# Kernel tuning notes

Hardware: AMD Instinct MI355X
Metric: run time of the kernel (lower is better)

Reference implementation:

```python
import jax, jax.numpy as jnp
import numpy as np

TAU = 1.0
EPS = 1e-5


def _gcn_sparse(x, src, dst, ew, W, b, n):
    # PyG GCNConv: add self-loops (weight 1), sym-normalize, aggregate src->dst
    deg = jax.ops.segment_sum(ew, dst, num_segments=n) + 1.0
    dinv = jnp.where(deg > 0, jax.lax.rsqrt(deg), 0.0)
    h = x @ W
    coef = dinv[src] * ew * dinv[dst]              # [E]
    out = jax.ops.segment_sum(h[src] * coef[:, None], dst, num_segments=n)
    out = out + h * (dinv * dinv)[:, None]         # self-loop term
    return out + b


def _gcn_dense(x, A, W, b):
    # x: [B,N,d], A: [B,N,N] with A[b,i,j] = weight of edge j->i
    n = A.shape[-1]
    Ah = A + jnp.eye(n, dtype=A.dtype)
    deg = Ah.sum(-1)
    dinv = jnp.where(deg > 0, jax.lax.rsqrt(deg), 0.0)
    An = dinv[:, :, None] * Ah * dinv[:, None, :]
    return jnp.einsum('bij,bjd->bid', An, x @ W) + b


def _bn_silu(x, g, be, axes):
    # BatchNorm over node axis (training-mode batch stats, biased var) + SiLU
    m = x.mean(axes, keepdims=True)
    v = x.var(axes, keepdims=True)
    return jax.nn.silu(g * (x - m) * jax.lax.rsqrt(v + EPS) + be)


def setup_inputs() -> dict:
    key = jax.random.key(0)
    ks = jax.random.split(key, 12)
    B, NPG, EPER = 32, 1024, 16384
    CIN, C, K1, K2, OUT = 64, 128, 128, 32, 10
    N, E = B * NPG, B * EPER
    ei = jax.random.randint(ks[0], (2, E), 0, NPG, dtype=jnp.int32)
    off = jnp.repeat(jnp.arange(B, dtype=jnp.int32) * NPG, EPER)
    edge_index = ei + off[None, :]
    x = jax.random.normal(ks[1], (N, CIN), jnp.float32)
    batch = jnp.repeat(jnp.arange(B, dtype=jnp.int32), NPG)
    batch_ptr = jnp.arange(B + 1, dtype=jnp.int32) * NPG
    p = lambda k, s: jax.random.normal(k, s, jnp.float32) * 0.05
    return dict(
        x=x, edge_index=edge_index, batch=batch, batch_ptr=batch_ptr,
        w1a=p(ks[2], (CIN, C)), b1a=jnp.zeros((C,)), g1a=jnp.ones((C,)), be1a=jnp.zeros((C,)),
        w1b=p(ks[3], (C, C)), b1b=jnp.zeros((C,)), g1b=jnp.ones((C,)), be1b=jnp.zeros((C,)),
        wp1=p(ks[4], (C, K1)), bp1=jnp.zeros((K1,)),
        w2a=p(ks[5], (C, C)), b2a=jnp.zeros((C,)), g2a=jnp.ones((C,)), be2a=jnp.zeros((C,)),
        w2b=p(ks[6], (C, C)), b2b=jnp.zeros((C,)), g2b=jnp.ones((C,)), be2b=jnp.zeros((C,)),
        wp2=p(ks[7], (C, K2)), bp2=jnp.zeros((K2,)),
        wl=p(ks[8], (C, OUT)), bl=jnp.zeros((OUT,)))


def reference(x, edge_index, batch, batch_ptr,
              w1a, b1a, g1a, be1a, w1b, b1b, g1b, be1b, wp1, bp1,
              w2a, b2a, g2a, be2a, w2b, b2b, g2b, be2b, wp2, bp2,
              wl, bl):
    n = x.shape[0]
    B = batch_ptr.shape[0] - 1
    npg = n // B                                    # uniform nodes per graph
    src, dst = edge_index[0], edge_index[1]
    ew = jnp.ones((edge_index.shape[1],), x.dtype)  # edge_weight=None -> ones

    # ---- stack 1: sparse GCN residual blocks + stochastic pool ----
    h = _bn_silu(_gcn_sparse(x, src, dst, ew, w1a, b1a, n), g1a, be1a, 0)
    h = h + _bn_silu(_gcn_sparse(h, src, dst, ew, w1b, b1b, n), g1b, be1b, 0)
    s = jax.nn.softmax(_gcn_sparse(h, src, dst, ew, wp1, bp1, n) / TAU, -1)  # [n,K1]
    s3 = s.reshape(B, npg, -1)
    x2 = jnp.einsum('bnc,bnd->bcd', s3, h.reshape(B, npg, -1))   # s^T x  [B,K1,C]
    t = jax.ops.segment_sum(s[src] * ew[:, None], dst, num_segments=n)  # A s
    A2 = jnp.einsum('bnc,bnk->bck', s3, t.reshape(B, npg, -1))   # s^T A s [B,K1,K1]

    # ---- stack 2: dense GCN on pooled graph + stochastic pool ----
    h2 = _bn_silu(_gcn_dense(x2, A2, w2a, b2a), g2a, be2a, (0, 1))
    h2 = h2 + _bn_silu(_gcn_dense(h2, A2, w2b, b2b), g2b, be2b, (0, 1))
    s2 = jax.nn.softmax(_gcn_dense(h2, A2, wp2, bp2) / TAU, -1)  # [B,K1,K2]
    x3 = jnp.einsum('bnc,bnd->bcd', s2, h2)                      # [B,K2,C]

    # global mean pool over nodes per graph, linear, log_softmax
    g = x3.mean(axis=1)
    out = jax.nn.log_softmax(g @ wl + bl, axis=1)
    # aux losses are multiplied by 0 in the original forward -> exact zero
    return (out, jnp.zeros((), x.dtype))
```

## Files before the change

kernel.cpp:

```cpp
#include <hip/hip_runtime.h>
#include <cmath>

#define KSPLIT 8
#define ELL_ST 80

typedef __attribute__((ext_vector_type(8))) short short8;
typedef __attribute__((ext_vector_type(4))) float float4v;

static __device__ __forceinline__ unsigned short f2bf(float f){
  union { float f; unsigned u; } c; c.f = f;
  unsigned r = c.u + 0x7fff + ((c.u >> 16) & 1);
  return (unsigned short)(r >> 16);
}
static __device__ __forceinline__ float u2f(unsigned u){
  union { unsigned u; float f; } c; c.u = u; return c.f;
}
static __device__ __forceinline__ float silu(float y){ return y/(1.f+__expf(-y)); }

static __device__ __forceinline__ void coef_prologue(const float* __restrict__ stats,
                                                     const float* __restrict__ gamma,
                                                     const float* __restrict__ beta,
                                                     float invM, float* lds, int tbase){
  int t = threadIdx.x - tbase;
  if(t >= 0 && t < 128){
    float s = 0.f, q = 0.f;
    #pragma unroll
    for(int k=0;k<8;k++){ s += stats[k*128+t]; q += stats[1024 + k*128+t]; }
    float m = s*invM;
    float v = q*invM - m*m;
    float sc = gamma[t]*rsqrtf(v + 1e-5f);
    lds[t] = sc;
    lds[128+t] = beta[t] - m*sc;
  }
}

__global__ void k_fill_ell(const int* __restrict__ src, const int* __restrict__ dst,
                           int* __restrict__ cursor, int* __restrict__ esrc, int E){
  int e = blockIdx.x*256 + threadIdx.x;
  if(e<E){
    int d = dst[e];
    int p = atomicAdd(&cursor[d], 1);
    if(p < ELL_ST) esrc[(size_t)d*ELL_ST + p] = src[e];
  }
}

__global__ void k_dinv_wt(const int* __restrict__ deg, float* __restrict__ dinv, int n,
                          const float* __restrict__ w1a, const float* __restrict__ w1b,
                          const float* __restrict__ wp1, unsigned short* __restrict__ t1a,
                          unsigned short* __restrict__ t1b, unsigned short* __restrict__ tp1,
                          int CIN){
  int i = blockIdx.x*256 + threadIdx.x;
  if(i < n){ dinv[i] = rsqrtf((float)deg[i] + 1.0f); }
  int j = i - n;
  int n1 = CIN*128, n2 = 128*128;
  if(j >= 0 && j < n1){
    int k = j >> 7, c = j & 127;
    t1a[(size_t)c*CIN + k] = f2bf(w1a[j]);
  } else if(j >= n1 && j < n1+n2){
    int jj = j - n1; int k = jj >> 7, c = jj & 127;
    t1b[(size_t)c*128 + k] = f2bf(w1b[jj]);
  } else if(j >= n1+n2 && j < n1+2*n2){
    int jj = j - n1 - n2; int k = jj >> 7, c = jj & 127;
    tp1[(size_t)c*128 + k] = f2bf(wp1[jj]);
  }
}

__global__ void k_gemm_mfma(const float* __restrict__ A, const float* __restrict__ A2,
                            const unsigned short* __restrict__ Bt,
                            unsigned short* __restrict__ Cb, int M, int K, int Nc,
                            const float* __restrict__ rowscale,
                            const float* __restrict__ stA, const float* __restrict__ gA,
                            const float* __restrict__ beA,
                            const float* __restrict__ stB, const float* __restrict__ gB,
                            const float* __restrict__ beB, float invM){
  __shared__ unsigned short Abf[64][40];
  __shared__ unsigned short Bbf[64][40];
  __shared__ float lcA[256], lcB[256];
  int tid = threadIdx.x;
  if(stA) coef_prologue(stA, gA, beA, invM, lcA, 0);
  if(stB) coef_prologue(stB, gB, beB, invM, lcB, 128);
  if(stA || stB) __syncthreads();
  int wv = tid >> 6, lane = tid & 63;
  int quad = lane >> 4, l16 = lane & 15;
  int row0 = blockIdx.y*64, col0 = blockIdx.x*64;
  int sr = tid >> 2, sk = (tid & 3)*8;
  float4v acc[4] = {};
  for(int kt=0; kt<K; kt+=32){
    const float* ap = &A[(size_t)(row0+sr)*K + kt + sk];
    float va[8];
    *(float4*)&va[0] = *(const float4*)ap;
    *(float4*)&va[4] = *(const float4*)(ap+4);
    if(stB){
      const float* bp = &A2[(size_t)(row0+sr)*K + kt + sk];
      float vb[8];
      *(float4*)&vb[0] = *(const float4*)bp;
      *(float4*)&vb[4] = *(const float4*)(bp+4);
      #pragma unroll
      for(int i=0;i<8;i++){
        int c = kt+sk+i;
        va[i] = silu(lcA[c]*va[i] + lcA[128+c]) + silu(lcB[c]*vb[i] + lcB[128+c]);
      }
    } else if(stA){
      #pragma unroll
      for(int i=0;i<8;i++){
        int c = kt+sk+i;
        va[i] = silu(lcA[c]*va[i] + lcA[128+c]);
      }
    }
    uint4 pk;
    pk.x = (unsigned)f2bf(va[0]) | ((unsigned)f2bf(va[1])<<16);
    pk.y = (unsigned)f2bf(va[2]) | ((unsigned)f2bf(va[3])<<16);
    pk.z = (unsigned)f2bf(va[4]) | ((unsigned)f2bf(va[5])<<16);
    pk.w = (unsigned)f2bf(va[6]) | ((unsigned)f2bf(va[7])<<16);
    *(uint4*)&Abf[sr][sk] = pk;
    *(uint4*)&Bbf[sr][sk] = *(const uint4*)&Bt[(size_t)(col0+sr)*K + kt + sk];
    __syncthreads();
    short8 af = *(const short8*)&Abf[wv*16 + l16][quad*8];
    #pragma unroll
    for(int t=0;t<4;t++){
      short8 bf = *(const short8*)&Bbf[t*16 + l16][quad*8];
      acc[t] = __builtin_amdgcn_mfma_f32_16x16x32_bf16(af, bf, acc[t], 0, 0, 0);
    }
    __syncthreads();
  }
  float scr[4];
  #pragma unroll
  for(int r=0;r<4;r++){
    int grow = row0 + wv*16 + quad*4 + r;
    scr[r] = rowscale ? rowscale[grow] : 1.f;
  }
  #pragma unroll
  for(int t=0;t<4;t++){
    #pragma unroll
    for(int r=0;r<4;r++){
      int grow = row0 + wv*16 + quad*4 + r;
      int gcol = col0 + t*16 + l16;
      Cb[(size_t)grow*Nc + gcol] = f2bf(acc[t][r]*scr[r]);
    }
  }
}

__global__ void k_gemm64(const float* __restrict__ A, const float* __restrict__ B,
                         float* __restrict__ C, int M, int K, int Nc,
                         const float* __restrict__ rowscale,
                         const float* __restrict__ stA, const float* __restrict__ gA,
                         const float* __restrict__ beA, float invM){
  __shared__ float As[16][68];
  __shared__ float Bs[16][68];
  __shared__ float lc[256];
  int tid = threadIdx.x;
  if(stA){ coef_prologue(stA, gA, beA, invM, lc, 0); __syncthreads(); }
  int tx = tid & 15, ty = tid >> 4;
  int row0 = blockIdx.y*64, col0 = blockIdx.x*64;
  float acc[4][4] = {};
  for(int kt=0; kt<K; kt+=16){
    int ra = tid >> 2, ka = (tid & 3)*4;
    float4 va = *(const float4*)&A[(size_t)(row0+ra)*K + kt + ka];
    if(stA){
      float vv[4] = {va.x, va.y, va.z, va.w};
      #pragma unroll
      for(int i=0;i<4;i++){
        int c = kt+ka+i;
        vv[i] = silu(lc[c]*vv[i] + lc[128+c]);
      }
      va.x=vv[0]; va.y=vv[1]; va.z=vv[2]; va.w=vv[3];
    }
    As[ka+0][ra]=va.x; As[ka+1][ra]=va.y; As[ka+2][ra]=va.z; As[ka+3][ra]=va.w;
    int rb = tid >> 4, cb = (tid & 15)*4;
    *(float4*)&Bs[rb][cb] = *(const float4*)&B[(size_t)(kt+rb)*Nc + col0 + cb];
    __syncthreads();
    #pragma unroll
    for(int k=0;k<16;k++){
      float4 a = *(const float4*)&As[k][ty*4];
      float4 b = *(const float4*)&Bs[k][tx*4];
      float av[4]={a.x,a.y,a.z,a.w}, bv[4]={b.x,b.y,b.z,b.w};
      #pragma unroll
      for(int i=0;i<4;i++)
        #pragma unroll
        for(int j=0;j<4;j++) acc[i][j] += av[i]*bv[j];
    }
    __syncthreads();
  }
  #pragma unroll
  for(int i=0;i<4;i++){
    int r = row0 + ty*4 + i;
    float sc = rowscale ? rowscale[r] : 1.0f;
    float4 v; v.x=acc[i][0]*sc; v.y=acc[i][1]*sc; v.z=acc[i][2]*sc; v.w=acc[i][3]*sc;
    *(float4*)&C[(size_t)r*Nc + col0 + tx*4] = v;
  }
}

template<bool DO_SOFTMAX, bool GCN, bool STATS, bool BF16IN>
__global__ void k_gather(const int* __restrict__ degc, const int* __restrict__ esrc,
                         const float* __restrict__ dinv, const void* __restrict__ hWs,
                         const float* __restrict__ bias, float* __restrict__ out,
                         float* __restrict__ stats){
  __shared__ float lsum[4][128];
  __shared__ float lsq[4][128];
  const unsigned short* h16 = (const unsigned short*)hWs;
  const float* h32 = (const float*)hWs;
  int wave = threadIdx.x >> 6;
  int lane = threadIdx.x & 63;
  int bid = blockIdx.x;
  int d = ((bid & 7) << 12) | ((bid >> 3) << 2) | wave;
  int grp = lane >> 5;
  int c4 = (lane & 31)*4;
  int cnt = degc[d]; if(cnt > ELL_ST) cnt = ELL_ST;
  cnt = __builtin_amdgcn_readfirstlane(cnt);
  const int* row = esrc + (size_t)d*ELL_ST;

  auto loadrow = [&](int s)->float4{
    if(BF16IN){
      uint2 u = *(const uint2*)&h16[(size_t)s*128 + c4];
      float4 v;
      v.x = u2f(u.x << 16); v.y = u2f(u.x & 0xffff0000u);
      v.z = u2f(u.y << 16); v.w = u2f(u.y & 0xffff0000u);
      return v;
    } else {
      return *(const float4*)&h32[(size_t)s*128 + c4];
    }
  };

  float4 a0 = {0.f,0.f,0.f,0.f}, a1 = {0.f,0.f,0.f,0.f};
  float4 a2 = {0.f,0.f,0.f,0.f}, a3 = {0.f,0.f,0.f,0.f};
  if(GCN && grp == 0)
    a0 = loadrow(d);
  for(int base=0; base<cnt; base+=32){
    int m = cnt - base; if(m > 32) m = 32;
    int idx = (lane < m) ? row[base + lane] : 0;
    int full = m & ~7;
    int j0 = 0;
    for(; j0 < full; j0 += 8){
      int s0 = __shfl(idx, j0+grp);
      int s1 = __shfl(idx, j0+grp+2);
      int s2 = __shfl(idx, j0+grp+4);
      int s3 = __shfl(idx, j0+grp+6);
      float4 v0 = loadrow(s0);
      float4 v1 = loadrow(s1);
      float4 v2 = loadrow(s2);
      float4 v3 = loadrow(s3);
      a0.x+=v0.x; a0.y+=v0.y; a0.z+=v0.z; a0.w+=v0.w;
      a1.x+=v1.x; a1.y+=v1.y; a1.z+=v1.z; a1.w+=v1.w;
      a2.x+=v2.x; a2.y+=v2.y; a2.z+=v2.z; a2.w+=v2.w;
      a3.x+=v3.x; a3.y+=v3.y; a3.z+=v3.z; a3.w+=v3.w;
    }
    if(j0 < m){
      int jj0 = j0+grp, jj1 = j0+grp+2, jj2 = j0+grp+4, jj3 = j0+grp+6;
      int s0 = __shfl(idx, jj0 < m ? jj0 : 0);
      int s1 = __shfl(idx, jj1 < m ? jj1 : 0);
      int s2 = __shfl(idx, jj2 < m ? jj2 : 0);
      int s3 = __shfl(idx, jj3 < m ? jj3 : 0);
      if(jj0 < m){ float4 v = loadrow(s0);
        a0.x+=v.x; a0.y+=v.y; a0.z+=v.z; a0.w+=v.w; }
      if(jj1 < m){ float4 v = loadrow(s1);
        a1.x+=v.x; a1.y+=v.y; a1.z+=v.z; a1.w+=v.w; }
      if(jj2 < m){ float4 v = loadrow(s2);
        a2.x+=v.x; a2.y+=v.y; a2.z+=v.z; a2.w+=v.w; }
      if(jj3 < m){ float4 v = loadrow(s3);
        a3.x+=v.x; a3.y+=v.y; a3.z+=v.z; a3.w+=v.w; }
    }
  }
  float4 acc;
  acc.x = (a0.x+a1.x)+(a2.x+a3.x);
  acc.y = (a0.y+a1.y)+(a2.y+a3.y);
  acc.z = (a0.z+a1.z)+(a2.z+a3.z);
  acc.w = (a0.w+a1.w)+(a2.w+a3.w);
  acc.x += __shfl_xor(acc.x, 32);
  acc.y += __shfl_xor(acc.y, 32);
  acc.z += __shfl_xor(acc.z, 32);
  acc.w += __shfl_xor(acc.w, 32);
  float4 val = acc;
  if(GCN){
    float dv = dinv[d];
    float4 bi = *(const float4*)&bias[c4];
    val.x = dv*acc.x + bi.x; val.y = dv*acc.y + bi.y;
    val.z = dv*acc.z + bi.z; val.w = dv*acc.w + bi.w;
  }
  if(DO_SOFTMAX){
    float mx = fmaxf(fmaxf(val.x,val.y), fmaxf(val.z,val.w));
    #pragma unroll
    for(int o=1;o<32;o<<=1) mx = fmaxf(mx, __shfl_xor(mx,o));
    float4 e; e.x=__expf(val.x-mx); e.y=__expf(val.y-mx);
    e.z=__expf(val.z-mx); e.w=__expf(val.w-mx);
    float s = e.x+e.y+e.z+e.w;
    #pragma unroll
    for(int o=1;o<32;o<<=1) s += __shfl_xor(s,o);
    float inv = 1.f/s;
    val.x=e.x*inv; val.y=e.y*inv; val.z=e.z*inv; val.w=e.w*inv;
  }
  if(grp == 0)
    *(float4*)&out[(size_t)d*128 + c4] = val;
  if(STATS){
    if(grp == 0){
      *(float4*)&lsum[wave][c4] = val;
      float4 q; q.x=val.x*val.x; q.y=val.y*val.y; q.z=val.z*val.z; q.w=val.w*val.w;
      *(float4*)&lsq[wave][c4] = q;
    }
    __syncthreads();
    int t = threadIdx.x;
    if(t < 128){
      float s = (lsum[0][t]+lsum[1][t]) + (lsum[2][t]+lsum[3][t]);
      atomicAdd(&stats[(bid & 7)*128 + t], s);
    } else {
      int c = t - 128;
      float q = (lsq[0][c]+lsq[1][c]) + (lsq[2][c]+lsq[3][c]);
      atomicAdd(&stats[1024 + (bid & 7)*128 + c], q);
    }
  }
}

__global__ __launch_bounds__(256, 2)
void k_pool2(const float* __restrict__ P, const float* __restrict__ Qa,
             const float* __restrict__ Qb, const float* __restrict__ Qc,
             const float* __restrict__ stA, const float* __restrict__ gA,
             const float* __restrict__ beA,
             const float* __restrict__ stB, const float* __restrict__ gB,
             const float* __restrict__ beB, float invM,
             float* __restrict__ part1, float* __restrict__ part2, int npg, int nb){
  __shared__ float Ps[2][8][132], Qs[2][8][132];
  __shared__ float lcA[256], lcB[256];
  int tid = threadIdx.x;
  bool fused = (blockIdx.z == 0);
  if(fused){
    coef_prologue(stA, gA, beA, invM, lcA, 0);
    coef_prologue(stB, gB, beB, invM, lcB, 128);
    __syncthreads();
  }
  int ks = blockIdx.x, b = blockIdx.y;
  int klen = npg / KSPLIT;
  size_t base = ((size_t)b*npg + (size_t)ks*klen)*128;
  int tx = tid & 15, ty = tid >> 4;
  int r = tid >> 5, c4s = (tid & 31)*4;
  size_t off = (size_t)r*128 + c4s;
  const float* Q1 = fused ? Qa : Qc;

  auto stage_q = [&](float4 qa, float4 qb)->float4{
    float4 q;
    if(fused){
      q.x = silu(lcA[c4s+0]*qa.x+lcA[128+c4s+0]) + silu(lcB[c4s+0]*qb.x+lcB[128+c4s+0]);
      q.y = silu(lcA[c4s+1]*qa.y+lcA[128+c4s+1]) + silu(lcB[c4s+1]*qb.y+lcB[128+c4s+1]);
      q.z = silu(lcA[c4s+2]*qa.z+lcA[128+c4s+2]) + silu(lcB[c4s+2]*qb.z+lcB[128+c4s+2]);
      q.w = silu(lcA[c4s+3]*qa.w+lcA[128+c4s+3]) + silu(lcB[c4s+3]*qb.w+lcB[128+c4s+3]);
    } else q = qa;
    return q;
  };

  {
    float4 p0 = *(const float4*)&P[base + off];
    float4 qa0 = *(const float4*)&Q1[base + off];
    float4 qb0 = fused ? *(const float4*)&Qb[base + off] : qa0;
    *(float4*)&Ps[0][r][c4s] = p0;
    *(float4*)&Qs[0][r][c4s] = stage_q(qa0, qb0);
  }
  __syncthreads();

  float acc[8][8] = {};
  int chunks = klen >> 3;
  for(int c=0; c<chunks; c++){
    float4 pn, qan, qbn;
    if(c+1 < chunks){
      size_t nb2 = base + (size_t)((c+1)*8)*128 + off;
      pn  = *(const float4*)&P[nb2];
      qan = *(const float4*)&Q1[nb2];
      if(fused) qbn = *(const float4*)&Qb[nb2];
    }
    int cb = c & 1;
    #pragma unroll
    for(int k=0;k<8;k++){
      float4 a0 = *(const float4*)&Ps[cb][k][ty*4];
      float4 a1 = *(const float4*)&Ps[cb][k][64+ty*4];
      float4 b0 = *(const float4*)&Qs[cb][k][tx*4];
      float4 b1 = *(const float4*)&Qs[cb][k][64+tx*4];
      float av[8]={a0.x,a0.y,a0.z,a0.w,a1.x,a1.y,a1.z,a1.w};
      float bv[8]={b0.x,b0.y,b0.z,b0.w,b1.x,b1.y,b1.z,b1.w};
      #pragma unroll
      for(int i=0;i<8;i++)
        #pragma unroll
        for(int j=0;j<8;j++) acc[i][j] += av[i]*bv[j];
    }
    if(c+1 < chunks){
      int nbuf = (c+1) & 1;
      *(float4*)&Ps[nbuf][r][c4s] = pn;
      *(float4*)&Qs[nbuf][r][c4s] = stage_q(qan, fused ? qbn : qan);
    }
    __syncthreads();
  }

  float* outp = (fused ? part1 : part2) + ((size_t)(ks*nb + b)*128)*128;
  #pragma unroll
  for(int ih=0; ih<2; ih++)
    #pragma unroll
    for(int ii=0; ii<4; ii++){
      int i = ih*64 + ty*4 + ii;
      #pragma unroll
      for(int jh=0; jh<2; jh++){
        float4 v;
        v.x = acc[ih*4+ii][jh*4+0];
        v.y = acc[ih*4+ii][jh*4+1];
        v.z = acc[ih*4+ii][jh*4+2];
        v.w = acc[ih*4+ii][jh*4+3];
        *(float4*)&outp[(size_t)i*128 + jh*64 + tx*4] = v;
      }
    }
}

__global__ void k_pool_reduce2(const float* __restrict__ p1, const float* __restrict__ p2,
                               float* __restrict__ x2, float* __restrict__ A2,
                               float* __restrict__ dinv2, int total){
  int i = blockIdx.x*256 + threadIdx.x;
  int half = total >> 2;
  if(i < half){
    float4 s = *(const float4*)&p1[(size_t)i*4];
    #pragma unroll
    for(int ks=1; ks<KSPLIT; ks++){
      float4 v = *(const float4*)&p1[(size_t)ks*total + (size_t)i*4];
      s.x+=v.x; s.y+=v.y; s.z+=v.z; s.w+=v.w;
    }
    *(float4*)&x2[(size_t)i*4] = s;
  } else {
    int ia = i - half;
    float4 s = *(const float4*)&p2[(size_t)ia*4];
    #pragma unroll
    for(int ks=1; ks<KSPLIT; ks++){
      float4 v = *(const float4*)&p2[(size_t)ks*total + (size_t)ia*4];
      s.x+=v.x; s.y+=v.y; s.z+=v.z; s.w+=v.w;
    }
    *(float4*)&A2[(size_t)ia*4] = s;
    float rs = s.x+s.y+s.z+s.w;
    #pragma unroll
    for(int o=16;o>0;o>>=1) rs += __shfl_xor(rs, o);
    if((threadIdx.x & 31) == 0) dinv2[ia>>5] = rsqrtf(rs + 1.0f);
  }
}

__global__ void k_bgemm_post_stats(const float* __restrict__ A, const float* __restrict__ X,
                                   const float* __restrict__ dinv2, const float* __restrict__ bias,
                                   float* __restrict__ outp, float* __restrict__ stats){
  __shared__ float As[16][17], Xs[16][17];
  __shared__ float rs[16][17], rq[16][17];
  int b = blockIdx.z;
  int i0 = blockIdx.y*16, j0 = blockIdx.x*16;
  int tx = threadIdx.x, ty = threadIdx.y;
  const float* Ab = A + (size_t)b*16384;
  const float* Xb = X + (size_t)b*16384;
  float acc = 0.f;
  for(int k0=0;k0<128;k0+=16){
    As[ty][tx] = Ab[(i0+ty)*128 + k0+tx];
    Xs[ty][tx] = Xb[(k0+ty)*128 + j0+tx];
    __syncthreads();
    #pragma unroll
    for(int k=0;k<16;k++) acc += As[ty][k]*Xs[k][tx];
    __syncthreads();
  }
  int gr = b*128 + i0 + ty;
  float v = dinv2[gr]*(acc + Xb[(i0+ty)*128 + j0+tx]) + bias[j0+tx];
  outp[(size_t)gr*128 + j0+tx] = v;
  rs[ty][tx] = v; rq[ty][tx] = v*v;
  __syncthreads();
  if(ty == 0){
    float s = 0.f, q = 0.f;
    #pragma unroll
    for(int k=0;k<16;k++){ s += rs[k][tx]; q += rq[k][tx]; }
    int slot = b & 7;
    atomicAdd(&stats[slot*128 + j0+tx], s);
    atomicAdd(&stats[1024 + slot*128 + j0+tx], q);
  }
}

__global__ void k_final_reduce(const float* __restrict__ dTa, const float* __restrict__ dTb,
                               const float* __restrict__ stA, const float* __restrict__ gA,
                               const float* __restrict__ beA,
                               const float* __restrict__ stB, const float* __restrict__ gB,
                               const float* __restrict__ beB, float invMc,
                               float* __restrict__ g, int K1n, int Cc, float inv_k2){
  __shared__ float red[256];
  __shared__ float lcA[256], lcB[256];
  coef_prologue(stA, gA, beA, invMc, lcA, 0);
  coef_prologue(stB, gB, beB, invMc, lcB, 128);
  __syncthreads();
  int b = blockIdx.y;
  int n0 = blockIdx.x*16;
  int tid = threadIdx.x;
  int c = tid & 127, rh = tid >> 7;
  const float* pa = dTa + ((size_t)b*K1n + n0)*Cc;
  const float* pb = dTb + ((size_t)b*K1n + n0)*Cc;
  float sa = lcA[c], ha = lcA[128+c], sb = lcB[c], hb = lcB[128+c];
  float acc = 0.f;
  for(int r = rh; r < 16; r += 2){
    float ya = sa*pa[(size_t)r*Cc + c] + ha;
    float yb = sb*pb[(size_t)r*Cc + c] + hb;
    acc += silu(ya) + silu(yb);
  }
  red[tid] = acc;
  __syncthreads();
  if(tid < 128)
    atomicAdd(&g[b*128 + c], (red[tid] + red[tid+128]) * inv_k2);
}

__global__ void k_final3(const float* __restrict__ g, const float* __restrict__ wl,
                         const float* __restrict__ bl, float* __restrict__ out,
                         int Cc, int OUTc, int zero_idx){
  int b = blockIdx.x;
  int t = threadIdx.x;
  __shared__ float logits[32];
  __shared__ float mred, lred;
  const float* gb = g + b*Cc;
  if(t < OUTc){
    float l = bl[t];
    for(int d=0; d<Cc; d++) l += gb[d]*wl[d*OUTc + t];
    logits[t] = l;
  }
  __syncthreads();
  if(t==0){
    float m = -1e30f;
    for(int o=0;o<OUTc;o++) m = fmaxf(m, logits[o]);
    float s = 0.f;
    for(int o=0;o<OUTc;o++) s += __expf(logits[o]-m);
    mred = m; lred = logf(s);
  }
  __syncthreads();
  if(t < OUTc) out[b*OUTc + t] = logits[t] - mred - lred;
  if(b==0 && t==0 && zero_idx >= 0) out[zero_idx] = 0.f;
}

extern "C" void kernel_launch(void* const* d_in, const int* in_sizes, int n_in,
                              void* d_out, int out_size, void* d_ws, size_t ws_size,
                              hipStream_t stream){
  const float* x    = (const float*)d_in[0];
  const int*   ei   = (const int*)d_in[1];
  const float* w1a  = (const float*)d_in[4];
  const float* b1a  = (const float*)d_in[5];
  const float* g1a  = (const float*)d_in[6];
  const float* be1a = (const float*)d_in[7];
  const float* w1b  = (const float*)d_in[8];
  const float* b1b  = (const float*)d_in[9];
  const float* g1b  = (const float*)d_in[10];
  const float* be1b = (const float*)d_in[11];
  const float* wp1  = (const float*)d_in[12];
  const float* bp1  = (const float*)d_in[13];
  const float* w2a  = (const float*)d_in[14];
  const float* b2a  = (const float*)d_in[15];
  const float* g2a  = (const float*)d_in[16];
  const float* be2a = (const float*)d_in[17];
  const float* w2b  = (const float*)d_in[18];
  const float* b2b  = (const float*)d_in[19];
  const float* g2b  = (const float*)d_in[20];
  const float* be2b = (const float*)d_in[21];
  const float* wl   = (const float*)d_in[24];
  const float* bl   = (const float*)d_in[25];
  float* out = (float*)d_out;

  const int C_   = in_sizes[5];
  const int CIN_ = in_sizes[4]/C_;
  const int N    = in_sizes[0]/CIN_;
  const int E    = in_sizes[1]/2;
  const int B_   = in_sizes[3]-1;
  const int NPG_ = N/B_;
  const int K1_  = in_sizes[13];
  const int K2_  = in_sizes[23];
  const int OUTc = in_sizes[25];
  const int M2   = B_*K1_;
  const int total = M2*C_;

  const int* srcI = ei;
  const int* dstI = ei + E;

  float* ws = (float*)d_ws;
  size_t o = 0;
  float* dinv  = ws + o; o += (size_t)N;
  unsigned short* bufW = (unsigned short*)(ws + o); o += (size_t)N*C_/2;
  float* bufA  = ws + o; o += (size_t)N*C_;
  float* bufB  = ws + o; o += (size_t)N*C_;
  float* bufS  = ws + o; o += (size_t)N*C_;
  float* bufT  = ws + o; o += (size_t)N*C_;
  float* x2    = ws + o; o += (size_t)total;
  float* A2    = ws + o; o += (size_t)total;
  float* dinv2 = ws + o; o += (size_t)M2;
  float* st1a  = ws + o; o += 2048;
  float* st1b  = ws + o; o += 2048;
  float* stDa  = ws + o; o += 2048;
  float* stDb  = ws + o; o += 2048;
  float* gbuf  = ws + o; o += (size_t)B_*C_;
  int* cursor  = (int*)(ws + o); o += (size_t)N;
  float* part  = ws + o; o += (size_t)KSPLIT*total;
  float* part2 = ws + o; o += (size_t)KSPLIT*total;
  float* dW  = part;
  float* dTa = part + (size_t)total;
  float* dTb = part + 2*(size_t)total;
  unsigned short* wt1a = (unsigned short*)(ws + o); o += (size_t)CIN_*C_/2 + 64;
  unsigned short* wt1b = (unsigned short*)(ws + o); o += (size_t)C_*C_/2 + 64;
  unsigned short* wtp1 = (unsigned short*)(ws + o); o += (size_t)C_*C_/2 + 64;
  int* esrc    = (int*)(ws + o); o += (size_t)N*ELL_ST;
  (void)ws_size; (void)n_in;

  dim3 blk256(256);
  dim3 gblk(16,16);
  auto g1 = [](int n){ return dim3((unsigned)((n+255)/256)); };
  const float invN = 1.0f/N, invM2 = 1.0f/M2;

  hipMemsetAsync(st1a, 0, (4*2048 + (size_t)B_*C_)*sizeof(float) + (size_t)N*sizeof(int), stream);
  k_fill_ell<<<g1(E), blk256, 0, stream>>>(srcI, dstI, cursor, esrc, E);
  k_dinv_wt<<<g1(N + CIN_*C_ + 2*C_*C_), blk256, 0, stream>>>(cursor, dinv, N,
      w1a, w1b, wp1, wt1a, wt1b, wtp1, CIN_);

  dim3 gath((unsigned)(N/4));

  k_gemm_mfma<<<dim3(C_/64, N/64), blk256, 0, stream>>>(x, nullptr, wt1a, bufW, N, CIN_, C_, dinv,
      nullptr, nullptr, nullptr, nullptr, nullptr, nullptr, 0.f);
  k_gather<false,true,true,true><<<gath, blk256, 0, stream>>>(cursor, esrc, dinv, bufW, b1a, bufA, st1a);

  k_gemm_mfma<<<dim3(C_/64, N/64), blk256, 0, stream>>>(bufA, nullptr, wt1b, bufW, N, C_, C_, dinv,
      st1a, g1a, be1a, nullptr, nullptr, nullptr, invN);
  k_gather<false,true,true,true><<<gath, blk256, 0, stream>>>(cursor, esrc, dinv, bufW, b1b, bufB, st1b);

  k_gemm_mfma<<<dim3(K1_/64, N/64), blk256, 0, stream>>>(bufA, bufB, wtp1, bufW, N, C_, K1_, dinv,
      st1a, g1a, be1a, st1b, g1b, be1b, invN);
  k_gather<true,true,false,true><<<gath, blk256, 0, stream>>>(cursor, esrc, dinv, bufW, bp1, bufS, nullptr);
  k_gather<false,false,false,false><<<gath, blk256, 0, stream>>>(cursor, esrc, nullptr, bufS, nullptr, bufT, nullptr);

  k_pool2<<<dim3(KSPLIT, B_, 2), blk256, 0, stream>>>(bufS, bufA, bufB, bufT,
      st1a, g1a, be1a, st1b, g1b, be1b, invN, part, part2, NPG_, B_);
  k_pool_reduce2<<<g1(total/2), blk256, 0, stream>>>(part, part2, x2, A2, dinv2, total);

  k_gemm64<<<dim3(C_/64, M2/64), blk256, 0, stream>>>(x2, w2a, dW, M2, C_, C_, dinv2,
      nullptr, nullptr, nullptr, 0.f);
  k_bgemm_post_stats<<<dim3(C_/16, K1_/16, B_), gblk, 0, stream>>>(A2, dW, dinv2, b2a, dTa, stDa);

  k_gemm64<<<dim3(C_/64, M2/64), blk256, 0, stream>>>(dTa, w2b, dW, M2, C_, C_, dinv2,
      stDa, g2a, be2a, invM2);
  k_bgemm_post_stats<<<dim3(C_/16, K1_/16, B_), gblk, 0, stream>>>(A2, dW, dinv2, b2b, dTb, stDb);

  int zero_idx = (out_size > B_*OUTc) ? B_*OUTc : -1;
  k_final_reduce<<<dim3(K1_/16, B_), blk256, 0, stream>>>(dTa, dTb,
      stDa, g2a, be2a, stDb, g2b, be2b, invM2, gbuf, K1_, C_, 1.0f/K2_);
  k_final3<<<dim3((unsigned)B_), dim3(128), 0, stream>>>(gbuf, wl, bl, out, C_, OUTc, zero_idx);
}
```

Measured before the change: 375.5 us.

## Store pooling assignment buffers in bf16 and fuse final reduce with classifier

The softmax assignment matrix S and its propagated product A·S are now written by the gather kernels as packed bf16 rather than fp32. The second gather and k_pool2 read them as bf16 and widen to float on load, halving traffic on these two N×128 buffers. The final reduction and the logits/log-softmax kernels are merged into one per-graph kernel, removing a launch, an atomic accumulation buffer and part of the memset. The bf16 rounding of the assignment values adds precision loss.

New measurement: 382.5 us. About the same (+1.9%).

```diff
diff --git a/kernel.cpp b/kernel.cpp
--- a/kernel.cpp
+++ b/kernel.cpp
@@ -190,7 +190,7 @@
   }
 }
 
-template<bool DO_SOFTMAX, bool GCN, bool STATS, bool BF16IN>
+template<bool DO_SOFTMAX, bool GCN, bool STATS, bool BF16IN, bool BF16OUT>
 __global__ void k_gather(const int* __restrict__ degc, const int* __restrict__ esrc,
                          const float* __restrict__ dinv, const void* __restrict__ hWs,
                          const float* __restrict__ bias, float* __restrict__ out,
@@ -288,8 +288,17 @@
     float inv = 1.f/s;
     val.x=e.x*inv; val.y=e.y*inv; val.z=e.z*inv; val.w=e.w*inv;
   }
-  if(grp == 0)
-    *(float4*)&out[(size_t)d*128 + c4] = val;
+  if(grp == 0){
+    if(BF16OUT){
+      unsigned short* o16 = (unsigned short*)out;
+      uint2 w;
+      w.x = (unsigned)f2bf(val.x) | ((unsigned)f2bf(val.y)<<16);
+      w.y = (unsigned)f2bf(val.z) | ((unsigned)f2bf(val.w)<<16);
+      *(uint2*)&o16[(size_t)d*128 + c4] = w;
+    } else {
+      *(float4*)&out[(size_t)d*128 + c4] = val;
+    }
+  }
   if(STATS){
     if(grp == 0){
       *(float4*)&lsum[wave][c4] = val;
@@ -310,8 +319,8 @@
 }
 
 __global__ __launch_bounds__(256, 2)
-void k_pool2(const float* __restrict__ P, const float* __restrict__ Qa,
-             const float* __restrict__ Qb, const float* __restrict__ Qc,
+void k_pool2(const unsigned short* __restrict__ P, const float* __restrict__ Qa,
+             const float* __restrict__ Qb, const unsigned short* __restrict__ Qc,
              const float* __restrict__ stA, const float* __restrict__ gA,
              const float* __restrict__ beA,
              const float* __restrict__ stB, const float* __restrict__ gB,
@@ -332,37 +341,51 @@
   int tx = tid & 15, ty = tid >> 4;
   int r = tid >> 5, c4s = (tid & 31)*4;
   size_t off = (size_t)r*128 + c4s;
-  const float* Q1 = fused ? Qa : Qc;
-
+
+  auto ldbf = [&](const unsigned short* p, size_t idx)->float4{
+    uint2 u = *(const uint2*)&p[idx];
+    float4 v;
+    v.x = u2f(u.x << 16); v.y = u2f(u.x & 0xffff0000u);
+    v.z = u2f(u.y << 16); v.w = u2f(u.y & 0xffff0000u);
+    return v;
+  };
   auto stage_q = [&](float4 qa, float4 qb)->float4{
     float4 q;
-    if(fused){
-      q.x = silu(lcA[c4s+0]*qa.x+lcA[128+c4s+0]) + silu(lcB[c4s+0]*qb.x+lcB[128+c4s+0]);
-      q.y = silu(lcA[c4s+1]*qa.y+lcA[128+c4s+1]) + silu(lcB[c4s+1]*qb.y+lcB[128+c4s+1]);
-      q.z = silu(lcA[c4s+2]*qa.z+lcA[128+c4s+2]) + silu(lcB[c4s+2]*qb.z+lcB[128+c4s+2]);
-      q.w = silu(lcA[c4s+3]*qa.w+lcA[128+c4s+3]) + silu(lcB[c4s+3]*qb.w+lcB[128+c4s+3]);
-    } else q = qa;
+    q.x = silu(lcA[c4s+0]*qa.x+lcA[128+c4s+0]) + silu(lcB[c4s+0]*qb.x+lcB[128+c4s+0]);
+    q.y = silu(lcA[c4s+1]*qa.y+lcA[128+c4s+1]) + silu(lcB[c4s+1]*qb.y+lcB[128+c4s+1]);
+    q.z = silu(lcA[c4s+2]*qa.z+lcA[128+c4s+2]) + silu(lcB[c4s+2]*qb.z+lcB[128+c4s+2]);
+    q.w = silu(lcA[c4s+3]*qa.w+lcA[128+c4s+3]) + silu(lcB[c4s+3]*qb.w+lcB[128+c4s+3]);
     return q;
   };
 
   {
-    float4 p0 = *(const float4*)&P[base + off];
-    float4 qa0 = *(const float4*)&Q1[base + off];
-    float4 qb0 = fused ? *(const float4*)&Qb[base + off] : qa0;
+    float4 p0 = ldbf(P, base + off);
+    float4 q0;
+    if(fused){
+      float4 qa0 = *(const float4*)&Qa[base + off];
+      float4 qb0 = *(const float4*)&Qb[base + off];
+      q0 = stage_q(qa0, qb0);
+    } else {
+      q0 = ldbf(Qc, base + off);
+    }
     *(float4*)&Ps[0][r][c4s] = p0;
-    *(float4*)&Qs[0][r][c4s] = stage_q(qa0, qb0);
+    *(float4*)&Qs[0][r][c4s] = q0;
   }
   __syncthreads();
 
   float acc[8][8] = {};
   int chunks = klen >> 3;
   for(int c=0; c<chunks; c++){
-    float4 pn, qan, qbn;
+    float4 pn, qan, qbn, qn;
     if(c+1 < chunks){
       size_t nb2 = base + (size_t)((c+1)*8)*128 + off;
-      pn  = *(const float4*)&P[nb2];
-      qan = *(const float4*)&Q1[nb2];
-      if(fused) qbn = *(const float4*)&Qb[nb2];
+      pn = ldbf(P, nb2);
+      if(fused){
+        qan = *(const float4*)&Qa[nb2];
+        qbn = *(const float4*)&Qb[nb2];
+      } else {
+        qn = ldbf(Qc, nb2);
+      }
     }
     int cb = c & 1;
     #pragma unroll
@@ -381,7 +404,7 @@
     if(c+1 < chunks){
       int nbuf = (c+1) & 1;
       *(float4*)&Ps[nbuf][r][c4s] = pn;
-      *(float4*)&Qs[nbuf][r][c4s] = stage_q(qan, fused ? qbn : qan);
+      *(float4*)&Qs[nbuf][r][c4s] = fused ? stage_q(qan, qbn) : qn;
     }
     __syncthreads();
   }
@@ -467,51 +490,45 @@
   }
 }
 
-__global__ void k_final_reduce(const float* __restrict__ dTa, const float* __restrict__ dTb,
-                               const float* __restrict__ stA, const float* __restrict__ gA,
-                               const float* __restrict__ beA,
-                               const float* __restrict__ stB, const float* __restrict__ gB,
-                               const float* __restrict__ beB, float invMc,
-                               float* __restrict__ g, int K1n, int Cc, float inv_k2){
+__global__ void k_final(const float* __restrict__ dTa, const float* __restrict__ dTb,
+                        const float* __restrict__ stA, const float* __restrict__ gA,
+                        const float* __restrict__ beA,
+                        const float* __restrict__ stB, const float* __restrict__ gB,
+                        const float* __restrict__ beB, float invMc,
+                        const float* __restrict__ wl, const float* __restrict__ bl,
+                        float* __restrict__ out, int K1n, int Cc, float inv_k2,
+                        int OUTc, int zero_idx){
+  __shared__ float lcA[256], lcB[256];
   __shared__ float red[256];
-  __shared__ float lcA[256], lcB[256];
+  __shared__ float gsh[128];
+  __shared__ float logits[32];
+  __shared__ float mred, lred;
   coef_prologue(stA, gA, beA, invMc, lcA, 0);
   coef_prologue(stB, gB, beB, invMc, lcB, 128);
   __syncthreads();
-  int b = blockIdx.y;
-  int n0 = blockIdx.x*16;
+  int b = blockIdx.x;
   int tid = threadIdx.x;
   int c = tid & 127, rh = tid >> 7;
-  const float* pa = dTa + ((size_t)b*K1n + n0)*Cc;
-  const float* pb = dTb + ((size_t)b*K1n + n0)*Cc;
+  const float* pa = dTa + (size_t)b*K1n*Cc;
+  const float* pb = dTb + (size_t)b*K1n*Cc;
   float sa = lcA[c], ha = lcA[128+c], sb = lcB[c], hb = lcB[128+c];
   float acc = 0.f;
-  for(int r = rh; r < 16; r += 2){
+  for(int r = rh; r < K1n; r += 2){
     float ya = sa*pa[(size_t)r*Cc + c] + ha;
     float yb = sb*pb[(size_t)r*Cc + c] + hb;
     acc += silu(ya) + silu(yb);
   }
   red[tid] = acc;
   __syncthreads();
-  if(tid < 128)
-    atomicAdd(&g[b*128 + c], (red[tid] + red[tid+128]) * inv_k2);
-}
-
-__global__ void k_final3(const float* __restrict__ g, const float* __restrict__ wl,
-                         const float* __restrict__ bl, float* __restrict__ out,
-                         int Cc, int OUTc, int zero_idx){
-  int b = blockIdx.x;
-  int t = threadIdx.x;
-  __shared__ float logits[32];
-  __shared__ float mred, lred;
-  const float* gb = g + b*Cc;
-  if(t < OUTc){
-    float l = bl[t];
-    for(int d=0; d<Cc; d++) l += gb[d]*wl[d*OUTc + t];
-    logits[t] = l;
-  }
+  if(tid < 128) gsh[tid] = (red[tid] + red[tid+128]) * inv_k2;
   __syncthreads();
-  if(t==0){
+  if(tid < OUTc){
+    float l = bl[tid];
+    for(int d=0; d<Cc; d++) l += gsh[d]*wl[d*OUTc + tid];
+    logits[tid] = l;
+  }
+  __syncthreads();
+  if(tid==0){
     float m = -1e30f;
     for(int o=0;o<OUTc;o++) m = fmaxf(m, logits[o]);
     float s = 0.f;
@@ -519,8 +536,8 @@
     mred = m; lred = logf(s);
   }
   __syncthreads();
-  if(t < OUTc) out[b*OUTc + t] = logits[t] - mred - lred;
-  if(b==0 && t==0 && zero_idx >= 0) out[zero_idx] = 0.f;
+  if(tid < OUTc) out[b*OUTc + tid] = logits[tid] - mred - lred;
+  if(b==0 && tid==0 && zero_idx >= 0) out[zero_idx] = 0.f;
 }
 
 extern "C" void kernel_launch(void* const* d_in, const int* in_sizes, int n_in,
@@ -571,8 +588,8 @@
   unsigned short* bufW = (unsigned short*)(ws + o); o += (size_t)N*C_/2;
   float* bufA  = ws + o; o += (size_t)N*C_;
   float* bufB  = ws + o; o += (size_t)N*C_;
-  float* bufS  = ws + o; o += (size_t)N*C_;
-  float* bufT  = ws + o; o += (size_t)N*C_;
+  unsigned short* bufS = (unsigned short*)(ws + o); o += (size_t)N*C_/2;
+  unsigned short* bufT = (unsigned short*)(ws + o); o += (size_t)N*C_/2;
   float* x2    = ws + o; o += (size_t)total;
   float* A2    = ws + o; o += (size_t)total;
   float* dinv2 = ws + o; o += (size_t)M2;
@@ -580,7 +597,6 @@
   float* st1b  = ws + o; o += 2048;
   float* stDa  = ws + o; o += 2048;
   float* stDb  = ws + o; o += 2048;
-  float* gbuf  = ws + o; o += (size_t)B_*C_;
   int* cursor  = (int*)(ws + o); o += (size_t)N;
   float* part  = ws + o; o += (size_t)KSPLIT*total;
   float* part2 = ws + o; o += (size_t)KSPLIT*total;
@@ -598,7 +614,7 @@
   auto g1 = [](int n){ return dim3((unsigned)((n+255)/256)); };
   const float invN = 1.0f/N, invM2 = 1.0f/M2;
 
-  hipMemsetAsync(st1a, 0, (4*2048 + (size_t)B_*C_)*sizeof(float) + (size_t)N*sizeof(int), stream);
+  hipMemsetAsync(st1a, 0, (size_t)4*2048*sizeof(float) + (size_t)N*sizeof(int), stream);
   k_fill_ell<<<g1(E), blk256, 0, stream>>>(srcI, dstI, cursor, esrc, E);
   k_dinv_wt<<<g1(N + CIN_*C_ + 2*C_*C_), blk256, 0, stream>>>(cursor, dinv, N,
       w1a, w1b, wp1, wt1a, wt1b, wtp1, CIN_);
@@ -607,16 +623,16 @@
 
   k_gemm_mfma<<<dim3(C_/64, N/64), blk256, 0, stream>>>(x, nullptr, wt1a, bufW, N, CIN_, C_, dinv,
       nullptr, nullptr, nullptr, nullptr, nullptr, nullptr, 0.f);
-  k_gather<false,true,true,true><<<gath, blk256, 0, stream>>>(cursor, esrc, dinv, bufW, b1a, bufA, st1a);
+  k_gather<false,true,true,true,false><<<gath, blk256, 0, stream>>>(cursor, esrc, dinv, bufW, b1a, bufA, st1a);
 
   k_gemm_mfma<<<dim3(C_/64, N/64), blk256, 0, stream>>>(bufA, nullptr, wt1b, bufW, N, C_, C_, dinv,
       st1a, g1a, be1a, nullptr, nullptr, nullptr, invN);
-  k_gather<false,true,true,true><<<gath, blk256, 0, stream>>>(cursor, esrc, dinv, bufW, b1b, bufB, st1b);
+  k_gather<false,true,true,true,false><<<gath, blk256, 0, stream>>>(cursor, esrc, dinv, bufW, b1b, bufB, st1b);
 
   k_gemm_mfma<<<dim3(K1_/64, N/64), blk256, 0, stream>>>(bufA, bufB, wtp1, bufW, N, C_, K1_, dinv,
       st1a, g1a, be1a, st1b, g1b, be1b, invN);
-  k_gather<true,true,false,true><<<gath, blk256, 0, stream>>>(cursor, esrc, dinv, bufW, bp1, bufS, nullptr);
-  k_gather<false,false,false,false><<<gath, blk256, 0, stream>>>(cursor, esrc, nullptr, bufS, nullptr, bufT, nullptr);
+  k_gather<true,true,false,true,true><<<gath, blk256, 0, stream>>>(cursor, esrc, dinv, bufW, bp1, (float*)bufS, nullptr);
+  k_gather<false,false,false,true,true><<<gath, blk256, 0, stream>>>(cursor, esrc, nullptr, bufS, nullptr, (float*)bufT, nullptr);
 
   k_pool2<<<dim3(KSPLIT, B_, 2), blk256, 0, stream>>>(bufS, bufA, bufB, bufT,
       st1a, g1a, be1a, st1b, g1b, be1b, invN, part, part2, NPG_, B_);
@@ -631,7 +647,7 @@
   k_bgemm_post_stats<<<dim3(C_/16, K1_/16, B_), gblk, 0, stream>>>(A2, dW, dinv2, b2b, dTb, stDb);
 
   int zero_idx = (out_size > B_*OUTc) ? B_*OUTc : -1;
-  k_final_reduce<<<dim3(K1_/16, B_), blk256, 0, stream>>>(dTa, dTb,
-      stDa, g2a, be2a, stDb, g2b, be2b, invM2, gbuf, K1_, C_, 1.0f/K2_);
-  k_final3<<<dim3((unsigned)B_), dim3(128), 0, stream>>>(gbuf, wl, bl, out, C_, OUTc, zero_idx);
-}
+  k_final<<<dim3((unsigned)B_), blk256, 0, stream>>>(dTa, dTb,
+      stDa, g2a, be2a, stDb, g2b, be2b, invM2, wl, bl, out, K1_, C_, 1.0f/K2_,
+      OUTc, zero_idx);
+}
```

## Fuse ELL fill with weight transpose, compute dinv inline, merge final kernels

Applied to the files above, without the earlier changes.

Merges the ELL fill and weight-transpose kernels into one launch and drops the separate dinv array: GEMM and gather kernels now compute rsqrt(deg+1) from the cursor counts directly. The two final kernels are merged into one per-graph block that does the reduction, the linear layer and log_softmax, which removes the atomics and the gbuf memset. The stack-2 fp32 GEMM tile shrinks from 64x64 to 32x32 to launch more blocks on the small pooled problem. The aim is fewer launches and less small-kernel overhead. In exchange, the final kernel now has only 32 blocks doing all the reduction, and the smaller GEMM tiles get less data reuse.

Measured after the change: 381.8 us. About the same (+1.7%).

```diff
diff --git a/kernel.cpp b/kernel.cpp
--- a/kernel.cpp
+++ b/kernel.cpp
@@ -34,41 +34,37 @@
   }
 }
 
-__global__ void k_fill_ell(const int* __restrict__ src, const int* __restrict__ dst,
-                           int* __restrict__ cursor, int* __restrict__ esrc, int E){
-  int e = blockIdx.x*256 + threadIdx.x;
-  if(e<E){
-    int d = dst[e];
-    int p = atomicAdd(&cursor[d], 1);
-    if(p < ELL_ST) esrc[(size_t)d*ELL_ST + p] = src[e];
-  }
-}
-
-__global__ void k_dinv_wt(const int* __restrict__ deg, float* __restrict__ dinv, int n,
+__global__ void k_fill_wt(const int* __restrict__ src, const int* __restrict__ dst,
+                          int* __restrict__ cursor, int* __restrict__ esrc, int E,
                           const float* __restrict__ w1a, const float* __restrict__ w1b,
                           const float* __restrict__ wp1, unsigned short* __restrict__ t1a,
                           unsigned short* __restrict__ t1b, unsigned short* __restrict__ tp1,
                           int CIN){
   int i = blockIdx.x*256 + threadIdx.x;
-  if(i < n){ dinv[i] = rsqrtf((float)deg[i] + 1.0f); }
-  int j = i - n;
-  int n1 = CIN*128, n2 = 128*128;
-  if(j >= 0 && j < n1){
-    int k = j >> 7, c = j & 127;
-    t1a[(size_t)c*CIN + k] = f2bf(w1a[j]);
-  } else if(j >= n1 && j < n1+n2){
-    int jj = j - n1; int k = jj >> 7, c = jj & 127;
-    t1b[(size_t)c*128 + k] = f2bf(w1b[jj]);
-  } else if(j >= n1+n2 && j < n1+2*n2){
-    int jj = j - n1 - n2; int k = jj >> 7, c = jj & 127;
-    tp1[(size_t)c*128 + k] = f2bf(wp1[jj]);
+  if(i < E){
+    int d = dst[i];
+    int p = atomicAdd(&cursor[d], 1);
+    if(p < ELL_ST) esrc[(size_t)d*ELL_ST + p] = src[i];
+  } else {
+    int j = i - E;
+    int n1 = CIN*128, n2 = 128*128;
+    if(j >= 0 && j < n1){
+      int k = j >> 7, c = j & 127;
+      t1a[(size_t)c*CIN + k] = f2bf(w1a[j]);
+    } else if(j >= n1 && j < n1+n2){
+      int jj = j - n1; int k = jj >> 7, c = jj & 127;
+      t1b[(size_t)c*128 + k] = f2bf(w1b[jj]);
+    } else if(j >= n1+n2 && j < n1+2*n2){
+      int jj = j - n1 - n2; int k = jj >> 7, c = jj & 127;
+      tp1[(size_t)c*128 + k] = f2bf(wp1[jj]);
+    }
   }
 }
 
 __global__ void k_gemm_mfma(const float* __restrict__ A, const float* __restrict__ A2,
                             const unsigned short* __restrict__ Bt,
                             unsigned short* __restrict__ Cb, int M, int K, int Nc,
-                            const float* __restrict__ rowscale,
+                            const int* __restrict__ rowdeg,
                             const float* __restrict__ stA, const float* __restrict__ gA,
                             const float* __restrict__ beA,
                             const float* __restrict__ stB, const float* __restrict__ gB,
@@ -127,7 +123,7 @@
   #pragma unroll
   for(int r=0;r<4;r++){
     int grow = row0 + wv*16 + quad*4 + r;
-    scr[r] = rowscale ? rowscale[grow] : 1.f;
+    scr[r] = rowdeg ? rsqrtf((float)rowdeg[grow] + 1.0f) : 1.f;
   }
   #pragma unroll
   for(int t=0;t<4;t++){
@@ -140,59 +136,52 @@
   }
 }
 
-__global__ void k_gemm64(const float* __restrict__ A, const float* __restrict__ B,
+__global__ void k_gemm32(const float* __restrict__ A, const float* __restrict__ B,
                          float* __restrict__ C, int M, int K, int Nc,
                          const float* __restrict__ rowscale,
                          const float* __restrict__ stA, const float* __restrict__ gA,
                          const float* __restrict__ beA, float invM){
-  __shared__ float As[16][68];
-  __shared__ float Bs[16][68];
+  __shared__ float As[16][33];
+  __shared__ float Bs[16][33];
   __shared__ float lc[256];
   int tid = threadIdx.x;
   if(stA){ coef_prologue(stA, gA, beA, invM, lc, 0); __syncthreads(); }
   int tx = tid & 15, ty = tid >> 4;
-  int row0 = blockIdx.y*64, col0 = blockIdx.x*64;
-  float acc[4][4] = {};
+  int row0 = blockIdx.y*32, col0 = blockIdx.x*32;
+  float acc[2][2] = {};
   for(int kt=0; kt<K; kt+=16){
-    int ra = tid >> 2, ka = (tid & 3)*4;
-    float4 va = *(const float4*)&A[(size_t)(row0+ra)*K + kt + ka];
+    int ra = tid >> 3, ka = (tid & 7)*2;
+    float2 va = *(const float2*)&A[(size_t)(row0+ra)*K + kt + ka];
     if(stA){
-      float vv[4] = {va.x, va.y, va.z, va.w};
-      #pragma unroll
-      for(int i=0;i<4;i++){
-        int c = kt+ka+i;
-        vv[i] = silu(lc[c]*vv[i] + lc[128+c]);
-      }
-      va.x=vv[0]; va.y=vv[1]; va.z=vv[2]; va.w=vv[3];
-    }
-    As[ka+0][ra]=va.x; As[ka+1][ra]=va.y; As[ka+2][ra]=va.z; As[ka+3][ra]=va.w;
-    int rb = tid >> 4, cb = (tid & 15)*4;
-    *(float4*)&Bs[rb][cb] = *(const float4*)&B[(size_t)(kt+rb)*Nc + col0 + cb];
+      va.x = silu(lc[kt+ka]*va.x + lc[128+kt+ka]);
+      va.y = silu(lc[kt+ka+1]*va.y + lc[128+kt+ka+1]);
+    }
+    As[ka][ra] = va.x; As[ka+1][ra] = va.y;
+    int rb = tid >> 4, cb = (tid & 15)*2;
+    float2 vb = *(const float2*)&B[(size_t)(kt+rb)*Nc + col0 + cb];
+    Bs[rb][cb] = vb.x; Bs[rb][cb+1] = vb.y;
     __syncthreads();
     #pragma unroll
     for(int k=0;k<16;k++){
-      float4 a = *(const float4*)&As[k][ty*4];
-      float4 b = *(const float4*)&Bs[k][tx*4];
-      float av[4]={a.x,a.y,a.z,a.w}, bv[4]={b.x,b.y,b.z,b.w};
-      #pragma unroll
-      for(int i=0;i<4;i++)
-        #pragma unroll
-        for(int j=0;j<4;j++) acc[i][j] += av[i]*bv[j];
+      float a0 = As[k][ty*2], a1 = As[k][ty*2+1];
+      float b0 = Bs[k][tx*2], b1 = Bs[k][tx*2+1];
+      acc[0][0] += a0*b0; acc[0][1] += a0*b1;
+      acc[1][0] += a1*b0; acc[1][1] += a1*b1;
     }
     __syncthreads();
   }
   #pragma unroll
-  for(int i=0;i<4;i++){
-    int r = row0 + ty*4 + i;
+  for(int i=0;i<2;i++){
+    int r = row0 + ty*2 + i;
     float sc = rowscale ? rowscale[r] : 1.0f;
-    float4 v; v.x=acc[i][0]*sc; v.y=acc[i][1]*sc; v.z=acc[i][2]*sc; v.w=acc[i][3]*sc;
-    *(float4*)&C[(size_t)r*Nc + col0 + tx*4] = v;
+    float2 v; v.x = acc[i][0]*sc; v.y = acc[i][1]*sc;
+    *(float2*)&C[(size_t)r*Nc + col0 + tx*2] = v;
   }
 }
 
 template<bool DO_SOFTMAX, bool GCN, bool STATS, bool BF16IN>
 __global__ void k_gather(const int* __restrict__ degc, const int* __restrict__ esrc,
-                         const float* __restrict__ dinv, const void* __restrict__ hWs,
+                         const void* __restrict__ hWs,
                          const float* __restrict__ bias, float* __restrict__ out,
                          float* __restrict__ stats){
   __shared__ float lsum[4][128];
@@ -205,7 +194,8 @@
   int d = ((bid & 7) << 12) | ((bid >> 3) << 2) | wave;
   int grp = lane >> 5;
   int c4 = (lane & 31)*4;
-  int cnt = degc[d]; if(cnt > ELL_ST) cnt = ELL_ST;
+  int dgr = degc[d];
+  int cnt = dgr > ELL_ST ? ELL_ST : dgr;
   cnt = __builtin_amdgcn_readfirstlane(cnt);
   const int* row = esrc + (size_t)d*ELL_ST;
 
@@ -271,7 +261,7 @@
   acc.w += __shfl_xor(acc.w, 32);
   float4 val = acc;
   if(GCN){
-    float dv = dinv[d];
+    float dv = rsqrtf((float)dgr + 1.0f);
     float4 bi = *(const float4*)&bias[c4];
     val.x = dv*acc.x + bi.x; val.y = dv*acc.y + bi.y;
     val.z = dv*acc.z + bi.z; val.w = dv*acc.w + bi.w;
@@ -467,51 +457,45 @@
   }
 }
 
-__global__ void k_final_reduce(const float* __restrict__ dTa, const float* __restrict__ dTb,
-                               const float* __restrict__ stA, const float* __restrict__ gA,
-                               const float* __restrict__ beA,
-                               const float* __restrict__ stB, const float* __restrict__ gB,
-                               const float* __restrict__ beB, float invMc,
-                               float* __restrict__ g, int K1n, int Cc, float inv_k2){
+__global__ void k_final(const float* __restrict__ dTa, const float* __restrict__ dTb,
+                        const float* __restrict__ stA, const float* __restrict__ gA,
+                        const float* __restrict__ beA,
+                        const float* __restrict__ stB, const float* __restrict__ gB,
+                        const float* __restrict__ beB, float invMc,
+                        const float* __restrict__ wl, const float* __restrict__ bl,
+                        float* __restrict__ out, int K1n, int Cc, float inv_k2,
+                        int OUTc, int zero_idx){
+  __shared__ float lcA[256], lcB[256];
   __shared__ float red[256];
-  __shared__ float lcA[256], lcB[256];
+  __shared__ float gsh[128];
+  __shared__ float logits[32];
+  __shared__ float mred, lred;
   coef_prologue(stA, gA, beA, invMc, lcA, 0);
   coef_prologue(stB, gB, beB, invMc, lcB, 128);
   __syncthreads();
-  int b = blockIdx.y;
-  int n0 = blockIdx.x*16;
+  int b = blockIdx.x;
   int tid = threadIdx.x;
   int c = tid & 127, rh = tid >> 7;
-  const float* pa = dTa + ((size_t)b*K1n + n0)*Cc;
-  const float* pb = dTb + ((size_t)b*K1n + n0)*Cc;
+  const float* pa = dTa + (size_t)b*K1n*Cc;
+  const float* pb = dTb + (size_t)b*K1n*Cc;
   float sa = lcA[c], ha = lcA[128+c], sb = lcB[c], hb = lcB[128+c];
   float acc = 0.f;
-  for(int r = rh; r < 16; r += 2){
+  for(int r = rh; r < K1n; r += 2){
     float ya = sa*pa[(size_t)r*Cc + c] + ha;
     float yb = sb*pb[(size_t)r*Cc + c] + hb;
     acc += silu(ya) + silu(yb);
   }
   red[tid] = acc;
   __syncthreads();
-  if(tid < 128)
-    atomicAdd(&g[b*128 + c], (red[tid] + red[tid+128]) * inv_k2);
-}
-
-__global__ void k_final3(const float* __restrict__ g, const float* __restrict__ wl,
-                         const float* __restrict__ bl, float* __restrict__ out,
-                         int Cc, int OUTc, int zero_idx){
-  int b = blockIdx.x;
-  int t = threadIdx.x;
-  __shared__ float logits[32];
-  __shared__ float mred, lred;
-  const float* gb = g + b*Cc;
-  if(t < OUTc){
-    float l = bl[t];
-    for(int d=0; d<Cc; d++) l += gb[d]*wl[d*OUTc + t];
-    logits[t] = l;
-  }
+  if(tid < 128) gsh[tid] = (red[tid] + red[tid+128]) * inv_k2;
   __syncthreads();
-  if(t==0){
+  if(tid < OUTc){
+    float l = bl[tid];
+    for(int d=0; d<Cc; d++) l += gsh[d]*wl[d*OUTc + tid];
+    logits[tid] = l;
+  }
+  __syncthreads();
+  if(tid==0){
     float m = -1e30f;
     for(int o=0;o<OUTc;o++) m = fmaxf(m, logits[o]);
     float s = 0.f;
@@ -519,8 +503,8 @@
     mred = m; lred = logf(s);
   }
   __syncthreads();
-  if(t < OUTc) out[b*OUTc + t] = logits[t] - mred - lred;
-  if(b==0 && t==0 && zero_idx >= 0) out[zero_idx] = 0.f;
+  if(tid < OUTc) out[b*OUTc + tid] = logits[tid] - mred - lred;
+  if(b==0 && tid==0 && zero_idx >= 0) out[zero_idx] = 0.f;
 }
 
 extern "C" void kernel_launch(void* const* d_in, const int* in_sizes, int n_in,
@@ -567,7 +551,6 @@
 
   float* ws = (float*)d_ws;
   size_t o = 0;
-  float* dinv  = ws + o; o += (size_t)N;
   unsigned short* bufW = (unsigned short*)(ws + o); o += (size_t)N*C_/2;
   float* bufA  = ws + o; o += (size_t)N*C_;
   float* bufB  = ws + o; o += (size_t)N*C_;
@@ -580,7 +563,6 @@
   float* st1b  = ws + o; o += 2048;
   float* stDa  = ws + o; o += 2048;
   float* stDb  = ws + o; o += 2048;
-  float* gbuf  = ws + o; o += (size_t)B_*C_;
   int* cursor  = (int*)(ws + o); o += (size_t)N;
   float* part  = ws + o; o += (size_t)KSPLIT*total;
   float* part2 = ws + o; o += (size_t)KSPLIT*total;
@@ -598,40 +580,39 @@
   auto g1 = [](int n){ return dim3((unsigned)((n+255)/256)); };
   const float invN = 1.0f/N, invM2 = 1.0f/M2;
 
-  hipMemsetAsync(st1a, 0, (4*2048 + (size_t)B_*C_)*sizeof(float) + (size_t)N*sizeof(int), stream);
-  k_fill_ell<<<g1(E), blk256, 0, stream>>>(srcI, dstI, cursor, esrc, E);
-  k_dinv_wt<<<g1(N + CIN_*C_ + 2*C_*C_), blk256, 0, stream>>>(cursor, dinv, N,
+  hipMemsetAsync(st1a, 0, (size_t)4*2048*sizeof(float) + (size_t)N*sizeof(int), stream);
+  k_fill_wt<<<g1(E + CIN_*C_ + 2*C_*C_), blk256, 0, stream>>>(srcI, dstI, cursor, esrc, E,
       w1a, w1b, wp1, wt1a, wt1b, wtp1, CIN_);
 
   dim3 gath((unsigned)(N/4));
 
-  k_gemm_mfma<<<dim3(C_/64, N/64), blk256, 0, stream>>>(x, nullptr, wt1a, bufW, N, CIN_, C_, dinv,
+  k_gemm_mfma<<<dim3(C_/64, N/64), blk256, 0, stream>>>(x, nullptr, wt1a, bufW, N, CIN_, C_, cursor,
       nullptr, nullptr, nullptr, nullptr, nullptr, nullptr, 0.f);
-  k_gather<false,true,true,true><<<gath, blk256, 0, stream>>>(cursor, esrc, dinv, bufW, b1a, bufA, st1a);
-
-  k_gemm_mfma<<<dim3(C_/64, N/64), blk256, 0, stream>>>(bufA, nullptr, wt1b, bufW, N, C_, C_, dinv,
+  k_gather<false,true,true,true><<<gath, blk256, 0, stream>>>(cursor, esrc, bufW, b1a, bufA, st1a);
+
+  k_gemm_mfma<<<dim3(C_/64, N/64), blk256, 0, stream>>>(bufA, nullptr, wt1b, bufW, N, C_, C_, cursor,
       st1a, g1a, be1a, nullptr, nullptr, nullptr, invN);
-  k_gather<false,true,true,true><<<gath, blk256, 0, stream>>>(cursor, esrc, dinv, bufW, b1b, bufB, st1b);
-
-  k_gemm_mfma<<<dim3(K1_/64, N/64), blk256, 0, stream>>>(bufA, bufB, wtp1, bufW, N, C_, K1_, dinv,
+  k_gather<false,true,true,true><<<gath, blk256, 0, stream>>>(cursor, esrc, bufW, b1b, bufB, st1b);
+
+  k_gemm_mfma<<<dim3(K1_/64, N/64), blk256, 0, stream>>>(bufA, bufB, wtp1, bufW, N, C_, K1_, cursor,
       st1a, g1a, be1a, st1b, g1b, be1b, invN);
-  k_gather<true,true,false,true><<<gath, blk256, 0, stream>>>(cursor, esrc, dinv, bufW, bp1, bufS, nullptr);
-  k_gather<false,false,false,false><<<gath, blk256, 0, stream>>>(cursor, esrc, nullptr, bufS, nullptr, bufT, nullptr);
+  k_gather<true,true,false,true><<<gath, blk256, 0, stream>>>(cursor, esrc, bufW, bp1, bufS, nullptr);
+  k_gather<false,false,false,false><<<gath, blk256, 0, stream>>>(cursor, esrc, bufS, nullptr, bufT, nullptr);
 
   k_pool2<<<dim3(KSPLIT, B_, 2), blk256, 0, stream>>>(bufS, bufA, bufB, bufT,
       st1a, g1a, be1a, st1b, g1b, be1b, invN, part, part2, NPG_, B_);
   k_pool_reduce2<<<g1(total/2), blk256, 0, stream>>>(part, part2, x2, A2, dinv2, total);
 
-  k_gemm64<<<dim3(C_/64, M2/64), blk256, 0, stream>>>(x2, w2a, dW, M2, C_, C_, dinv2,
+  k_gemm32<<<dim3(C_/32, M2/32), blk256, 0, stream>>>(x2, w2a, dW, M2, C_, C_, dinv2,
       nullptr, nullptr, nullptr, 0.f);
   k_bgemm_post_stats<<<dim3(C_/16, K1_/16, B_), gblk, 0, stream>>>(A2, dW, dinv2, b2a, dTa, stDa);
 
-  k_gemm64<<<dim3(C_/64, M2/64), blk256, 0, stream>>>(dTa, w2b, dW, M2, C_, C_, dinv2,
+  k_gemm32<<<dim3(C_/32, M2/32), blk256, 0, stream>>>(dTa, w2b, dW, M2, C_, C_, dinv2,
       stDa, g2a, be2a, invM2);
   k_bgemm_post_stats<<<dim3(C_/16, K1_/16, B_), gblk, 0, stream>>>(A2, dW, dinv2, b2b, dTb, stDb);
 
   int zero_idx = (out_size > B_*OUTc) ? B_*OUTc : -1;
-  k_final_reduce<<<dim3(K1_/16, B_), blk256, 0, stream>>>(dTa, dTb,
-      stDa, g2a, be2a, stDb, g2b, be2b, invM2, gbuf, K1_, C_, 1.0f/K2_);
-  k_final3<<<dim3((unsigned)B_), dim3(128), 0, stream>>>(gbuf, wl, bl, out, C_, OUTc, zero_idx);
-}
+  k_final<<<dim3((unsigned)B_), blk256, 0, stream>>>(dTa, dTb,
+      stDa, g2a, be2a, stDb, g2b, be2b, invM2, wl, bl, out, K1_, C_, 1.0f/K2_,
+      OUTc, zero_idx);
+}
```
